# Kernel optimization log

Measured on AMD Instinct MI355X. Metric: run time of the kernel, lower is better.

## Reference

```python
import jax, jax.numpy as jnp
import numpy as np

NUM_USERS = 100000
NUM_ITEMS = 100000
H = 64          # hidden_dim
NH = 4          # num_heads
B, L, K = 256, 50, 100


def setup_inputs() -> dict:
    key = jax.random.key(0)
    ks = jax.random.split(key, 20)
    s = 0.02
    inp = {
        "user_ids": jax.random.randint(ks[0], (B,), 0, NUM_USERS),
        "item_ids": jax.random.randint(ks[1], (B,), 0, NUM_ITEMS),
        "history": jax.random.randint(ks[2], (B, L), 0, NUM_ITEMS),
        "neighbor_emb": jax.random.normal(ks[3], (B, L, K, H), dtype=jnp.float32),
        # parameters ([in,out] convention)
        "user_table": jax.random.normal(ks[4], (NUM_USERS, H), dtype=jnp.float32) * s,
        "item_table": jax.random.normal(ks[5], (NUM_ITEMS, H), dtype=jnp.float32) * s,
        "Wa": jax.random.normal(ks[6], (2 * H, 96), dtype=jnp.float32) * s,
        "ba": jnp.zeros((96,), jnp.float32),
        "W1": jax.random.normal(ks[7], (96, 48), dtype=jnp.float32) * s,
        "b1": jnp.zeros((48,), jnp.float32),
        "W2": jax.random.normal(ks[8], (48, 16), dtype=jnp.float32) * s,
        "b2": jnp.zeros((16,), jnp.float32),
        "W3": jax.random.normal(ks[9], (16, 1), dtype=jnp.float32) * s,
        "b3": jnp.zeros((1,), jnp.float32),
        "Wh": jax.random.normal(ks[10], (NH, H, H // NH), dtype=jnp.float32) * s,  # per-head proj
        "bh": jnp.zeros((NH, H // NH), jnp.float32),
        "Wf1": jax.random.normal(ks[11], (2 * H, H), dtype=jnp.float32) * s,
        "bf1": jnp.zeros((H,), jnp.float32),
        "Wo": jax.random.normal(ks[12], (H, 1), dtype=jnp.float32) * s,
        "bo": jnp.zeros((1,), jnp.float32),
    }
    return inp


def reference(user_ids, item_ids, history, neighbor_emb,
              user_table, item_table, Wa, ba, W1, b1, W2, b2, W3, b3,
              Wh, bh, Wf1, bf1, Wo, bo):
    user_emb = user_table[user_ids]                 # [B,H]
    item_emb = item_table[item_ids]                 # [B,H] (computed but unused, as in source)
    history_emb = item_table[history]               # [B,L,H]

    # expand history over K neighbors and concat with neighbor embeddings
    hist_exp = jnp.broadcast_to(history_emb[:, :, None, :], (B, L, K, H))
    attn_in = jnp.concatenate([hist_exp, neighbor_emb], axis=-1)  # [B,L,K,2H]

    # attention layer + small MLP -> per-edge logits
    h = jax.nn.relu(attn_in @ Wa + ba)              # [B,L,K,96]
    h = jax.nn.relu(h @ W1 + b1)                    # [B,L,K,48]
    h = jax.nn.relu(h @ W2 + b2)                    # [B,L,K,16]
    logits = (h @ W3 + b3)[..., 0]                  # [B,L,K]

    w = jax.nn.softmax(logits, axis=-1)             # softmax over neighbors
    agg = jnp.einsum('blk,blkh->blh', w, neighbor_emb)  # [B,L,H]

    # per-head projections, concat -> [B,L,H]
    heads = jnp.einsum('blh,nhd->blnd', agg, Wh) + bh
    agg = heads.reshape(B, L, H)

    agg = agg.mean(axis=1)                          # [B,H]

    combined = jnp.concatenate([user_emb, agg], axis=-1)  # [B,2H]
    combined = jax.nn.relu(combined @ Wf1 + bf1)    # dropout is identity in eval
    out = jax.nn.sigmoid(combined @ Wo + bo)        # [B,1]
    return out[:, 0]
```

## Files before the change

kernel.cpp:

```cpp
#include <hip/hip_runtime.h>
#include <hip/hip_bf16.h>
#include <math.h>

#define NB 256
#define NL 50
#define NK 100
#define NHID 64
#define NBL (NB * NL)

typedef __attribute__((ext_vector_type(8))) short short8;
typedef __attribute__((ext_vector_type(4))) short short4_t;
typedef __attribute__((ext_vector_type(4))) float floatx4;

#define ZSTRIDE 208

__device__ __forceinline__ short f2bf(float f) {
    __hip_bfloat16 h = __float2bfloat16(f);
    return *reinterpret_cast<short*>(&h);
}

__global__ __launch_bounds__(256) void pack_kernel(
    const float* __restrict__ Wa, const float* __restrict__ W1,
    const float* __restrict__ W2,
    short* __restrict__ WaP, short* __restrict__ W1P, short* __restrict__ W2P)
{
    int t = blockIdx.x * 256 + threadIdx.x;
    int stride = gridDim.x * 256;
    for (int s = t; s < 24 * 64; s += stride) {
        int l = s & 63, fi = s >> 6, n = fi >> 2, tk = fi & 3;
        int col = n * 16 + (l & 15);
        for (int j = 0; j < 8; ++j) {
            int k = tk * 32 + ((l >> 4) * 8) + j;
            WaP[s * 8 + j] = f2bf(Wa[k * 96 + col]);
        }
    }
    for (int s = t; s < 9 * 64; s += stride) {
        int l = s & 63, nt = s >> 6, n = nt / 3, tk = nt % 3;
        int col = n * 16 + (l & 15);
        for (int j = 0; j < 8; ++j) {
            int k = tk * 32 + ((l >> 4) * 8) + j;
            W1P[s * 8 + j] = f2bf(W1[k * 48 + col]);
        }
    }
    for (int s = t; s < 2 * 64; s += stride) {
        int l = s & 63, tk = s >> 6;
        int col = l & 15;
        for (int j = 0; j < 8; ++j) {
            int k = tk * 32 + ((l >> 4) * 8) + j;
            W2P[s * 8 + j] = (k < 48) ? f2bf(W2[k * 16 + col]) : (short)0;
        }
    }
}

__global__ __launch_bounds__(256) void edge_kernel(
    const int* __restrict__ history,
    const float* __restrict__ neighbor,
    const float* __restrict__ item_table,
    const float* __restrict__ b1v, const float* __restrict__ b2,
    const float* __restrict__ W3, const float* __restrict__ b3,
    const short* __restrict__ WaP, const short* __restrict__ W1P,
    const short* __restrict__ W2P,
    float* __restrict__ part)
{
    const int bl  = blockIdx.x;
    const int tid = threadIdx.x;
    const int wv  = tid >> 6;
    const int ln  = tid & 63;
    const int lr  = ln & 15;
    const int lg  = ln >> 4;

    __shared__ __align__(16) char z_s[7][16 * ZSTRIDE];
    __shared__ float logit_s[112];
    const int mi1 = wv + 4;
    const bool hasB = (mi1 < 7);
    char* zpA = z_s[wv];
    char* zpB = z_s[hasB ? mi1 : wv];

    const float* nbg = neighbor + (size_t)bl * (NK * NHID);

    const int hid = history[bl];
    const float* hbase = item_table + (size_t)hid * NHID;
    short8 h0, h1;
    {
        float4 u0 = *reinterpret_cast<const float4*>(hbase + lg * 8);
        float4 u1 = *reinterpret_cast<const float4*>(hbase + lg * 8 + 4);
        float4 u2 = *reinterpret_cast<const float4*>(hbase + 32 + lg * 8);
        float4 u3 = *reinterpret_cast<const float4*>(hbase + 32 + lg * 8 + 4);
        h0[0] = f2bf(u0.x); h0[1] = f2bf(u0.y); h0[2] = f2bf(u0.z); h0[3] = f2bf(u0.w);
        h0[4] = f2bf(u1.x); h0[5] = f2bf(u1.y); h0[6] = f2bf(u1.z); h0[7] = f2bf(u1.w);
        h1[0] = f2bf(u2.x); h1[1] = f2bf(u2.y); h1[2] = f2bf(u2.z); h1[3] = f2bf(u2.w);
        h1[4] = f2bf(u3.x); h1[5] = f2bf(u3.y); h1[6] = f2bf(u3.z); h1[7] = f2bf(u3.w);
    }

    const int er0 = wv * 16 + lr;
    const int er1 = mi1 * 16 + lr;
    const int ec1 = (er1 > NK - 1) ? NK - 1 : er1;
    const float* arow0 = nbg + er0 * NHID + lg * 8;
    const float* arow1 = nbg + ec1 * NHID + lg * 8;
    short8 a0, a1, a2, a3;
    {
        float4 f0 = *reinterpret_cast<const float4*>(arow0);
        float4 f1 = *reinterpret_cast<const float4*>(arow0 + 4);
        float4 f2 = *reinterpret_cast<const float4*>(arow0 + 32);
        float4 f3 = *reinterpret_cast<const float4*>(arow0 + 36);
        a0[0] = f2bf(f0.x); a0[1] = f2bf(f0.y); a0[2] = f2bf(f0.z); a0[3] = f2bf(f0.w);
        a0[4] = f2bf(f1.x); a0[5] = f2bf(f1.y); a0[6] = f2bf(f1.z); a0[7] = f2bf(f1.w);
        a1[0] = f2bf(f2.x); a1[1] = f2bf(f2.y); a1[2] = f2bf(f2.z); a1[3] = f2bf(f2.w);
        a1[4] = f2bf(f3.x); a1[5] = f2bf(f3.y); a1[6] = f2bf(f3.z); a1[7] = f2bf(f3.w);
    }
    if (hasB) {
        float4 f0 = *reinterpret_cast<const float4*>(arow1);
        float4 f1 = *reinterpret_cast<const float4*>(arow1 + 4);
        float4 f2 = *reinterpret_cast<const float4*>(arow1 + 32);
        float4 f3 = *reinterpret_cast<const float4*>(arow1 + 36);
        a2[0] = f2bf(f0.x); a2[1] = f2bf(f0.y); a2[2] = f2bf(f0.z); a2[3] = f2bf(f0.w);
        a2[4] = f2bf(f1.x); a2[5] = f2bf(f1.y); a2[6] = f2bf(f1.z); a2[7] = f2bf(f1.w);
        a3[0] = f2bf(f2.x); a3[1] = f2bf(f2.y); a3[2] = f2bf(f2.z); a3[3] = f2bf(f2.w);
        a3[4] = f2bf(f3.x); a3[5] = f2bf(f3.y); a3[6] = f2bf(f3.z); a3[7] = f2bf(f3.w);
    }

    const short8* WaPv = reinterpret_cast<const short8*>(WaP);
    const short8* W1Pv = reinterpret_cast<const short8*>(W1P);
    const short8* W2Pv = reinterpret_cast<const short8*>(W2P);
    const float b3s = b3[0];
    const floatx4 b2v = *reinterpret_cast<const floatx4*>(b2 + lg * 4);
    const floatx4 w3v = *reinterpret_cast<const floatx4*>(W3 + lg * 4);

    auto l1_stage = [&](char* zp, short8 b0, short8 b1) {
        #pragma unroll
        for (int t = 0; t < 6; ++t) {
            floatx4 acc = {0.f, 0.f, 0.f, 0.f};
            acc = __builtin_amdgcn_mfma_f32_16x16x32_bf16(WaPv[(t * 4 + 0) * 64 + ln], h0, acc, 0, 0, 0);
            acc = __builtin_amdgcn_mfma_f32_16x16x32_bf16(WaPv[(t * 4 + 1) * 64 + ln], h1, acc, 0, 0, 0);
            acc = __builtin_amdgcn_mfma_f32_16x16x32_bf16(WaPv[(t * 4 + 2) * 64 + ln], b0, acc, 0, 0, 0);
            acc = __builtin_amdgcn_mfma_f32_16x16x32_bf16(WaPv[(t * 4 + 3) * 64 + ln], b1, acc, 0, 0, 0);
            short4_t v;
            #pragma unroll
            for (int i = 0; i < 4; ++i) v[i] = f2bf(fmaxf(acc[i], 0.f));
            *reinterpret_cast<short4_t*>(zp + lr * ZSTRIDE + t * 32 + lg * 8) = v;
        }
    };
    auto l2_stage = [&](char* zp) {
        short8 za0 = *reinterpret_cast<const short8*>(zp + lr * ZSTRIDE +   0 + lg * 16);
        short8 za1 = *reinterpret_cast<const short8*>(zp + lr * ZSTRIDE +  64 + lg * 16);
        short8 za2 = *reinterpret_cast<const short8*>(zp + lr * ZSTRIDE + 128 + lg * 16);
        #pragma unroll
        for (int t = 0; t < 3; ++t) {
            floatx4 acc = {0.f, 0.f, 0.f, 0.f};
            acc = __builtin_amdgcn_mfma_f32_16x16x32_bf16(W1Pv[(t * 3 + 0) * 64 + ln], za0, acc, 0, 0, 0);
            acc = __builtin_amdgcn_mfma_f32_16x16x32_bf16(W1Pv[(t * 3 + 1) * 64 + ln], za1, acc, 0, 0, 0);
            acc = __builtin_amdgcn_mfma_f32_16x16x32_bf16(W1Pv[(t * 3 + 2) * 64 + ln], za2, acc, 0, 0, 0);
            floatx4 bb = *reinterpret_cast<const floatx4*>(b1v + t * 16 + lg * 4);
            short4_t v;
            #pragma unroll
            for (int i = 0; i < 4; ++i) v[i] = f2bf(fmaxf(acc[i] + bb[i], 0.f));
            *reinterpret_cast<short4_t*>(zp + lr * ZSTRIDE + t * 32 + lg * 8) = v;
        }
    };
    auto l3_stage = [&](char* zp, int mi) {
        short8 zb0 = *reinterpret_cast<const short8*>(zp + lr * ZSTRIDE + lg * 16);
        short8 zb1 = short8{0, 0, 0, 0, 0, 0, 0, 0};
        if (lg < 2)
            zb1 = *reinterpret_cast<const short8*>(zp + lr * ZSTRIDE + 64 + lg * 16);
        floatx4 c3 = {0.f, 0.f, 0.f, 0.f};
        c3 = __builtin_amdgcn_mfma_f32_16x16x32_bf16(W2Pv[ln], zb0, c3, 0, 0, 0);
        c3 = __builtin_amdgcn_mfma_f32_16x16x32_bf16(W2Pv[64 + ln], zb1, c3, 0, 0, 0);
        float p = 0.f;
        #pragma unroll
        for (int i = 0; i < 4; ++i)
            p += fmaxf(c3[i] + b2v[i], 0.f) * w3v[i];
        p += __shfl_xor(p, 16, 64);
        p += __shfl_xor(p, 32, 64);
        if (lg == 0 && mi * 16 + lr < NK) logit_s[mi * 16 + lr] = p + b3s;
    };

    l1_stage(zpA, a0, a1);
    if (hasB) l1_stage(zpB, a2, a3);
    l2_stage(zpA);
    if (hasB) l2_stage(zpB);
    l3_stage(zpA, wv);
    if (hasB) l3_stage(zpB, mi1);
    __syncthreads();

    float l0 = logit_s[ln];
    float l1 = (ln < NK - 64) ? logit_s[64 + ln] : -1e30f;
    float m = fmaxf(l0, l1);
    #pragma unroll
    for (int off = 32; off > 0; off >>= 1) m = fmaxf(m, __shfl_xor(m, off, 64));
    float p0 = __expf(l0 - m);
    float p1 = (ln < NK - 64) ? __expf(l1 - m) : 0.f;
    float s = p0 + p1;
    #pragma unroll
    for (int off = 32; off > 0; off >>= 1) s += __shfl_xor(s, off, 64);
    float inv = 1.f / s;
    float w0 = p0 * inv;
    float w1 = p1 * inv;

    float a = 0.f;
    #pragma unroll
    for (int kk = 0; kk < 25; ++kk) {
        int k = wv * 25 + kk;
        float wk = __shfl((k < 64) ? w0 : w1, k & 63, 64);
        a += wk * nbg[k * NHID + ln];
    }
    part[((size_t)bl * 4 + wv) * NHID + ln] = a;
}

__global__ __launch_bounds__(256) void final_kernel(
    const int* __restrict__ user_ids,
    const float* __restrict__ user_table,
    const float* __restrict__ part,
    const float* __restrict__ Wh, const float* __restrict__ bh,
    const float* __restrict__ Wf1, const float* __restrict__ bf1,
    const float* __restrict__ Wo,  const float* __restrict__ bo,
    float* __restrict__ out)
{
    const int b = blockIdx.x, tid = threadIdx.x;
    const int q = tid >> 6, h = tid & 63;
    __shared__ float red[4][64];
    __shared__ float ue[64], agm[64], agh[64];

    {
        float sum = 0.f;
        const float* pb = part + ((size_t)b * NL * 4 + q) * NHID + h;
        #pragma unroll 5
        for (int i = 0; i < NL; ++i)
            sum += pb[(size_t)i * 4 * NHID];
        red[q][h] = sum;
    }
    if (q == 0) {
        const int uid = user_ids[b];
        ue[h] = user_table[(size_t)uid * 64 + h];
    }
    __syncthreads();
    if (q == 0)
        agm[h] = (red[0][h] + red[1][h] + red[2][h] + red[3][h]) * (1.f / 50.f);
    __syncthreads();
    if (q == 0) {
        const int n = h >> 4, d = h & 15;
        float hv = bh[h];
        #pragma unroll 4
        for (int i = 0; i < 64; ++i)
            hv += agm[i] * Wh[n * (64 * 16) + i * 16 + d];
        agh[h] = hv;
    }
    __syncthreads();
    if (q == 0) {
        float z = bf1[h];
        #pragma unroll 4
        for (int i = 0; i < 64; ++i) z += ue[i] * Wf1[i * 64 + h];
        #pragma unroll 4
        for (int i = 0; i < 64; ++i) z += agh[i] * Wf1[(64 + i) * 64 + h];
        float t = fmaxf(z, 0.f) * Wo[h];
        #pragma unroll
        for (int off = 32; off > 0; off >>= 1) t += __shfl_down(t, off, 64);
        if (h == 0) out[b] = 1.f / (1.f + __expf(-(t + bo[0])));
    }
}

extern "C" void kernel_launch(void* const* d_in, const int* in_sizes, int n_in,
                              void* d_out, int out_size, void* d_ws, size_t ws_size,
                              hipStream_t stream) {
    const int*   user_ids   = (const int*)d_in[0];
    const int*   history    = (const int*)d_in[2];
    const float* neighbor   = (const float*)d_in[3];
    const float* user_table = (const float*)d_in[4];
    const float* item_table = (const float*)d_in[5];
    const float* Wa  = (const float*)d_in[6];
    const float* W1  = (const float*)d_in[8];
    const float* b1  = (const float*)d_in[9];
    const float* W2  = (const float*)d_in[10];
    const float* b2  = (const float*)d_in[11];
    const float* W3  = (const float*)d_in[12];
    const float* b3  = (const float*)d_in[13];
    const float* Wh  = (const float*)d_in[14];
    const float* bh  = (const float*)d_in[15];
    const float* Wf1 = (const float*)d_in[16];
    const float* bf1 = (const float*)d_in[17];
    const float* Wo  = (const float*)d_in[18];
    const float* bo  = (const float*)d_in[19];

    char* ws = (char*)d_ws;
    short* WaP  = (short*)(ws);
    short* W1P  = (short*)(ws + 24576);
    short* W2P  = (short*)(ws + 33792);
    float* part = (float*)(ws + 36864);

    pack_kernel<<<64, 256, 0, stream>>>(Wa, W1, W2, WaP, W1P, W2P);
    edge_kernel<<<NBL, 256, 0, stream>>>(history, neighbor, item_table,
        b1, b2, W3, b3, WaP, W1P, W2P, part);
    final_kernel<<<NB, 256, 0, stream>>>(user_ids, user_table, part, Wh, bh,
                                         Wf1, bf1, Wo, bo, (float*)d_out);
}
```

Before: 196.8 us.

## Make edge kernel persistent with register double-buffered prefetch of next row

The edge kernel now runs a fixed grid of 1024 blocks that stride over all batch-history rows instead of one block per row. While it computes the MLP and softmax for the current row, it prefetches the next row's history embedding and neighbor tiles into registers. An extra barrier guards logit_s reuse across iterations. This aims to hide global load latency and reduce block launch overhead, at the cost of higher register pressure (24 float4 buffers) and possibly lower occupancy.

```diff
diff --git a/kernel.cpp b/kernel.cpp
--- a/kernel.cpp
+++ b/kernel.cpp
@@ -7,6 +7,7 @@
 #define NK 100
 #define NHID 64
 #define NBL (NB * NL)
+#define EGRID 1024
 
 typedef __attribute__((ext_vector_type(8))) short short8;
 typedef __attribute__((ext_vector_type(4))) short short4_t;
@@ -62,7 +63,6 @@
     const short* __restrict__ W2P,
     float* __restrict__ part)
 {
-    const int bl  = blockIdx.x;
     const int tid = threadIdx.x;
     const int wv  = tid >> 6;
     const int ln  = tid & 63;
@@ -76,49 +76,6 @@
     char* zpA = z_s[wv];
     char* zpB = z_s[hasB ? mi1 : wv];
 
-    const float* nbg = neighbor + (size_t)bl * (NK * NHID);
-
-    const int hid = history[bl];
-    const float* hbase = item_table + (size_t)hid * NHID;
-    short8 h0, h1;
-    {
-        float4 u0 = *reinterpret_cast<const float4*>(hbase + lg * 8);
-        float4 u1 = *reinterpret_cast<const float4*>(hbase + lg * 8 + 4);
-        float4 u2 = *reinterpret_cast<const float4*>(hbase + 32 + lg * 8);
-        float4 u3 = *reinterpret_cast<const float4*>(hbase + 32 + lg * 8 + 4);
-        h0[0] = f2bf(u0.x); h0[1] = f2bf(u0.y); h0[2] = f2bf(u0.z); h0[3] = f2bf(u0.w);
-        h0[4] = f2bf(u1.x); h0[5] = f2bf(u1.y); h0[6] = f2bf(u1.z); h0[7] = f2bf(u1.w);
-        h1[0] = f2bf(u2.x); h1[1] = f2bf(u2.y); h1[2] = f2bf(u2.z); h1[3] = f2bf(u2.w);
-        h1[4] = f2bf(u3.x); h1[5] = f2bf(u3.y); h1[6] = f2bf(u3.z); h1[7] = f2bf(u3.w);
-    }
-
-    const int er0 = wv * 16 + lr;
-    const int er1 = mi1 * 16 + lr;
-    const int ec1 = (er1 > NK - 1) ? NK - 1 : er1;
-    const float* arow0 = nbg + er0 * NHID + lg * 8;
-    const float* arow1 = nbg + ec1 * NHID + lg * 8;
-    short8 a0, a1, a2, a3;
-    {
-        float4 f0 = *reinterpret_cast<const float4*>(arow0);
-        float4 f1 = *reinterpret_cast<const float4*>(arow0 + 4);
-        float4 f2 = *reinterpret_cast<const float4*>(arow0 + 32);
-        float4 f3 = *reinterpret_cast<const float4*>(arow0 + 36);
-        a0[0] = f2bf(f0.x); a0[1] = f2bf(f0.y); a0[2] = f2bf(f0.z); a0[3] = f2bf(f0.w);
-        a0[4] = f2bf(f1.x); a0[5] = f2bf(f1.y); a0[6] = f2bf(f1.z); a0[7] = f2bf(f1.w);
-        a1[0] = f2bf(f2.x); a1[1] = f2bf(f2.y); a1[2] = f2bf(f2.z); a1[3] = f2bf(f2.w);
-        a1[4] = f2bf(f3.x); a1[5] = f2bf(f3.y); a1[6] = f2bf(f3.z); a1[7] = f2bf(f3.w);
-    }
-    if (hasB) {
-        float4 f0 = *reinterpret_cast<const float4*>(arow1);
-        float4 f1 = *reinterpret_cast<const float4*>(arow1 + 4);
-        float4 f2 = *reinterpret_cast<const float4*>(arow1 + 32);
-        float4 f3 = *reinterpret_cast<const float4*>(arow1 + 36);
-        a2[0] = f2bf(f0.x); a2[1] = f2bf(f0.y); a2[2] = f2bf(f0.z); a2[3] = f2bf(f0.w);
-        a2[4] = f2bf(f1.x); a2[5] = f2bf(f1.y); a2[6] = f2bf(f1.z); a2[7] = f2bf(f1.w);
-        a3[0] = f2bf(f2.x); a3[1] = f2bf(f2.y); a3[2] = f2bf(f2.z); a3[3] = f2bf(f2.w);
-        a3[4] = f2bf(f3.x); a3[5] = f2bf(f3.y); a3[6] = f2bf(f3.z); a3[7] = f2bf(f3.w);
-    }
-
     const short8* WaPv = reinterpret_cast<const short8*>(WaP);
     const short8* W1Pv = reinterpret_cast<const short8*>(W1P);
     const short8* W2Pv = reinterpret_cast<const short8*>(W2P);
@@ -126,7 +83,36 @@
     const floatx4 b2v = *reinterpret_cast<const floatx4*>(b2 + lg * 4);
     const floatx4 w3v = *reinterpret_cast<const floatx4*>(W3 + lg * 4);
 
-    auto l1_stage = [&](char* zp, short8 b0, short8 b1) {
+    const int er0 = wv * 16 + lr;
+    const int er1 = mi1 * 16 + lr;
+    const int ec1 = (er1 > NK - 1) ? NK - 1 : er1;
+
+    auto load_bl = [&](int bl, float4* buf) {
+        const float* hb = item_table + (size_t)history[bl] * NHID;
+        buf[0] = *reinterpret_cast<const float4*>(hb + lg * 8);
+        buf[1] = *reinterpret_cast<const float4*>(hb + lg * 8 + 4);
+        buf[2] = *reinterpret_cast<const float4*>(hb + 32 + lg * 8);
+        buf[3] = *reinterpret_cast<const float4*>(hb + 32 + lg * 8 + 4);
+        const float* nb = neighbor + (size_t)bl * (NK * NHID);
+        const float* rA = nb + er0 * NHID + lg * 8;
+        buf[4] = *reinterpret_cast<const float4*>(rA);
+        buf[5] = *reinterpret_cast<const float4*>(rA + 4);
+        buf[6] = *reinterpret_cast<const float4*>(rA + 32);
+        buf[7] = *reinterpret_cast<const float4*>(rA + 36);
+        const float* rB = nb + ec1 * NHID + lg * 8;
+        buf[8]  = *reinterpret_cast<const float4*>(rB);
+        buf[9]  = *reinterpret_cast<const float4*>(rB + 4);
+        buf[10] = *reinterpret_cast<const float4*>(rB + 32);
+        buf[11] = *reinterpret_cast<const float4*>(rB + 36);
+    };
+    auto cvt8 = [](float4 x, float4 y) {
+        short8 r;
+        r[0] = f2bf(x.x); r[1] = f2bf(x.y); r[2] = f2bf(x.z); r[3] = f2bf(x.w);
+        r[4] = f2bf(y.x); r[5] = f2bf(y.y); r[6] = f2bf(y.z); r[7] = f2bf(y.w);
+        return r;
+    };
+
+    auto l1_stage = [&](char* zp, short8 h0, short8 h1, short8 b0, short8 b1) {
         #pragma unroll
         for (int t = 0; t < 6; ++t) {
             floatx4 acc = {0.f, 0.f, 0.f, 0.f};
@@ -174,36 +160,53 @@
         if (lg == 0 && mi * 16 + lr < NK) logit_s[mi * 16 + lr] = p + b3s;
     };
 
-    l1_stage(zpA, a0, a1);
-    if (hasB) l1_stage(zpB, a2, a3);
-    l2_stage(zpA);
-    if (hasB) l2_stage(zpB);
-    l3_stage(zpA, wv);
-    if (hasB) l3_stage(zpB, mi1);
-    __syncthreads();
-
-    float l0 = logit_s[ln];
-    float l1 = (ln < NK - 64) ? logit_s[64 + ln] : -1e30f;
-    float m = fmaxf(l0, l1);
-    #pragma unroll
-    for (int off = 32; off > 0; off >>= 1) m = fmaxf(m, __shfl_xor(m, off, 64));
-    float p0 = __expf(l0 - m);
-    float p1 = (ln < NK - 64) ? __expf(l1 - m) : 0.f;
-    float s = p0 + p1;
-    #pragma unroll
-    for (int off = 32; off > 0; off >>= 1) s += __shfl_xor(s, off, 64);
-    float inv = 1.f / s;
-    float w0 = p0 * inv;
-    float w1 = p1 * inv;
-
-    float a = 0.f;
-    #pragma unroll
-    for (int kk = 0; kk < 25; ++kk) {
-        int k = wv * 25 + kk;
-        float wk = __shfl((k < 64) ? w0 : w1, k & 63, 64);
-        a += wk * nbg[k * NHID + ln];
-    }
-    part[((size_t)bl * 4 + wv) * NHID + ln] = a;
+    float4 cur[12], nxt[12];
+    if (blockIdx.x < NBL) load_bl(blockIdx.x, cur);
+
+    for (int bl = blockIdx.x; bl < NBL; bl += EGRID) {
+        short8 h0 = cvt8(cur[0], cur[1]),  h1 = cvt8(cur[2], cur[3]);
+        short8 a0 = cvt8(cur[4], cur[5]),  a1 = cvt8(cur[6], cur[7]);
+        short8 a2 = cvt8(cur[8], cur[9]),  a3 = cvt8(cur[10], cur[11]);
+
+        const int nbl = bl + EGRID;
+        if (nbl < NBL) load_bl(nbl, nxt);
+
+        l1_stage(zpA, h0, h1, a0, a1);
+        if (hasB) l1_stage(zpB, h0, h1, a2, a3);
+        l2_stage(zpA);
+        if (hasB) l2_stage(zpB);
+        l3_stage(zpA, wv);
+        if (hasB) l3_stage(zpB, mi1);
+        __syncthreads();
+
+        float l0 = logit_s[ln];
+        float l1 = (ln < NK - 64) ? logit_s[64 + ln] : -1e30f;
+        __syncthreads();
+        float m = fmaxf(l0, l1);
+        #pragma unroll
+        for (int off = 32; off > 0; off >>= 1) m = fmaxf(m, __shfl_xor(m, off, 64));
+        float p0 = __expf(l0 - m);
+        float p1 = (ln < NK - 64) ? __expf(l1 - m) : 0.f;
+        float s = p0 + p1;
+        #pragma unroll
+        for (int off = 32; off > 0; off >>= 1) s += __shfl_xor(s, off, 64);
+        float inv = 1.f / s;
+        float w0 = p0 * inv;
+        float w1 = p1 * inv;
+
+        const float* nbg = neighbor + (size_t)bl * (NK * NHID);
+        float a = 0.f;
+        #pragma unroll
+        for (int kk = 0; kk < 25; ++kk) {
+            int k = wv * 25 + kk;
+            float wk = __shfl((k < 64) ? w0 : w1, k & 63, 64);
+            a += wk * nbg[k * NHID + ln];
+        }
+        part[((size_t)bl * 4 + wv) * NHID + ln] = a;
+
+        #pragma unroll
+        for (int i = 0; i < 12; ++i) cur[i] = nxt[i];
+    }
 }
 
 __global__ __launch_bounds__(256) void final_kernel(
@@ -287,7 +290,7 @@
     float* part = (float*)(ws + 36864);
 
     pack_kernel<<<64, 256, 0, stream>>>(Wa, W1, W2, WaP, W1P, W2P);
-    edge_kernel<<<NBL, 256, 0, stream>>>(history, neighbor, item_table,
+    edge_kernel<<<EGRID, 256, 0, stream>>>(history, neighbor, item_table,
         b1, b2, W3, b3, WaP, W1P, W2P, part);
     final_kernel<<<NB, 256, 0, stream>>>(user_ids, user_table, part, Wh, bh,
                                          Wf1, bf1, Wo, bo, (float*)d_out);
```

New measurement: 392.1 us. 1.99x slower.
